# Optimization experiments

Hardware: AMD Instinct MI355X
Metric: run time of the kernel (lower is better)

The kernel has to match this reference:

```python
import jax, jax.numpy as jnp
import numpy as np

P = 8      # patch_size
DIM = 16   # per-head channel dim
HEADS = 4
LN_EPS = 1e-6


def _conv_patch(x, W, b):
    # stride=kernel=P patch conv; SAME degenerates to VALID when H%P==0
    y = jax.lax.conv_general_dilated(
        x, W, window_strides=(P, P), padding='VALID',
        dimension_numbers=('NHWC', 'HWIO', 'NHWC'))
    return y + b


def _proj_heads(x, W, b):
    # b h w (c p0 p1 head) -> b head (h p0) (w p1) c
    y = _conv_patch(x, W, b)
    B, hh, ww, _ = y.shape
    y = y.reshape(B, hh, ww, DIM, P, P, HEADS)
    y = y.transpose(0, 6, 1, 4, 2, 5, 3)            # b head hh p0 ww p1 c
    return y.reshape(B, HEADS, hh * P, ww * P, DIM)


def _to_patch(t):
    # n head (h p1) (w p2) c -> n head c h w p1 p2
    B, hd, H, W, c = t.shape
    t = t.reshape(B, hd, H // P, P, W // P, P, c)
    return t.transpose(0, 1, 6, 2, 4, 3, 5)


def _from_patch(t):
    # n head c h w p1 p2 -> n head (h p1) (w p2) c
    B, hd, c, hh, ww, _, _ = t.shape
    t = t.transpose(0, 1, 3, 5, 4, 6, 2)
    return t.reshape(B, hd, hh * P, ww * P, c)


def setup_inputs() -> dict:
    key = jax.random.key(0)
    ks = jax.random.split(key, 6)
    B, H, W, Cin = 4, 256, 256, 16
    feat = DIM * HEADS * P * P  # 4096
    s_qkv = 0.02
    inp = {
        'x': jax.random.normal(ks[0], (B, H, W, Cin), jnp.float32),
        'Wq': jax.random.normal(ks[1], (P, P, Cin, feat), jnp.float32) * s_qkv,
        'bq': jnp.zeros((feat,), jnp.float32),
        'Wk': jax.random.normal(ks[2], (P, P, Cin, feat), jnp.float32) * s_qkv,
        'bk': jnp.zeros((feat,), jnp.float32),
        'Wv': jax.random.normal(ks[3], (P, P, Cin, feat), jnp.float32) * s_qkv,
        'bv': jnp.zeros((feat,), jnp.float32),
        'ln_scale': jnp.ones((DIM,), jnp.float32),
        'ln_bias': jnp.zeros((DIM,), jnp.float32),
        'Wout': jax.random.normal(ks[4], (P, P, HEADS * DIM, DIM * P * P), jnp.float32) * 0.02,
        'bout': jnp.zeros((DIM * P * P,), jnp.float32),
    }
    return inp


def reference(x, Wq, bq, Wk, bk, Wv, bv, ln_scale, ln_bias, Wout, bout):
    q = _proj_heads(x, Wq, bq)  # [B, heads, H, W, dim]
    k = _proj_heads(x, Wk, bk)
    v = _proj_heads(x, Wv, bv)

    # frequency-domain 'attention': per-8x8-patch rfft2 multiply irfft2
    qf = jnp.fft.rfft2(_to_patch(q))
    kf = jnp.fft.rfft2(_to_patch(k))
    out = jnp.fft.irfft2(qf * kf, s=(P, P))
    out = _from_patch(out)                          # [B, heads, H, W, dim]

    # LayerNorm over channel dim (flax default eps=1e-6, scale+bias)
    mu = out.mean(-1, keepdims=True)
    var = ((out - mu) ** 2).mean(-1, keepdims=True)
    out = (out - mu) * jax.lax.rsqrt(var + LN_EPS) * ln_scale + ln_bias

    out = v * out
    # b head h w c -> b h w (head c)
    B, hd, H, W, c = out.shape
    out = out.transpose(0, 2, 3, 1, 4).reshape(B, H, W, hd * c)

    # output projection (no heads): conv then b h w (c p0 p1) -> b (h p0) (w p1) c
    y = _conv_patch(out, Wout, bout)
    Bo, hh, ww, _ = y.shape
    y = y.reshape(Bo, hh, ww, DIM, P, P).transpose(0, 1, 4, 2, 5, 3)
    return y.reshape(Bo, hh * P, ww * P, DIM)
```

## Files before the change

### kernel.cpp

```cpp
#include <hip/hip_runtime.h>
#include <hip/hip_bf16.h>
#include <cstdint>
#include <cstddef>

typedef float  f32x4  __attribute__((ext_vector_type(4)));
typedef __bf16 bf16x8 __attribute__((ext_vector_type(8)));
typedef __bf16 bf16x4 __attribute__((ext_vector_type(4)));


#define GLOAD_LDS16(gp, lp)                                                     \
    __builtin_amdgcn_global_load_lds(                                           \
        (const __attribute__((address_space(1))) void*)(gp),                    \
        (__attribute__((address_space(3))) void*)(lp), 16, 0, 0)

__global__ __launch_bounds__(256) void k_im2col(const float* __restrict__ x,
                                                __bf16* __restrict__ Xb)
{
    const int p = blockIdx.x;
    const int t = threadIdx.x;
    const int b = p >> 10, hh = (p >> 5) & 31, ww = p & 31;
    const int e = t * 4;
    const int c = e & 15, ij = e >> 4;
    const int i = ij >> 3, j = ij & 7;
    const size_t src = ((((size_t)(b * 256 + hh * 8 + i)) * 256) + (ww * 8 + j)) * 16 + c;
    f32x4 v = *(const f32x4*)(x + src);
    bf16x4 o;
    o[0] = (__bf16)v[0]; o[1] = (__bf16)v[1]; o[2] = (__bf16)v[2]; o[3] = (__bf16)v[3];
    *(bf16x4*)(Xb + (size_t)p * 1024 + e) = o;
}

__global__ __launch_bounds__(256) void k_wqkvT(const float* __restrict__ Wq,
                                               const float* __restrict__ Wk,
                                               const float* __restrict__ Wv,
                                               __bf16* __restrict__ WT)
{
    __shared__ float tile[64][129];
    int q = blockIdx.x;
    const int t = threadIdx.x;
    const int k0 = (q & 7) * 128;  q >>= 3;
    const int ch = q & 15;         q >>= 4;
    const int head = q & 3;
    const int s = q >> 2;
    const float* __restrict__ W = (s == 0) ? Wq : (s == 1) ? Wk : Wv;

#pragma unroll
    for (int rep = 0; rep < 32; rep++) {
        const int idx = rep * 256 + t;
        const int kl = idx >> 6, pp = idx & 63;
        tile[pp][kl] = W[(size_t)(k0 + kl) * 4096 + ch * 256 + pp * 4 + head];
    }
    __syncthreads();
    const size_t nbase = (size_t)s * 4096 + head * 1024 + ch * 64;
#pragma unroll
    for (int rep = 0; rep < 32; rep++) {
        const int idx = rep * 256 + t;
        const int pp = idx >> 7, kl = idx & 127;
        WT[(nbase + pp) * 1024 + k0 + kl] = (__bf16)tile[pp][kl];
    }
}

__global__ __launch_bounds__(256) void k_biasperm(const float* __restrict__ bq,
                                                  const float* __restrict__ bk,
                                                  const float* __restrict__ bv,
                                                  float* __restrict__ bp)
{
    const int n = blockIdx.x * 256 + threadIdx.x;
    const int s = n >> 12;
    const int r = n & 4095;
    const int head = r >> 10, c = (r >> 6) & 15, pp = r & 63;
    const float* __restrict__ b = (s == 0) ? bq : (s == 1) ? bk : bv;
    bp[n] = b[c * 256 + pp * 4 + head];
}

__global__ __launch_bounds__(256) void k_woutT(const float* __restrict__ Wo,
                                               __bf16* __restrict__ WT)
{
    __shared__ float tile[64][129];
    const int q = blockIdx.x;
    const int t = threadIdx.x;
    const int n0 = (q & 15) * 64;
    const int k0 = (q >> 4) * 128;
    const int ch = n0 >> 6;
#pragma unroll
    for (int rep = 0; rep < 32; rep++) {
        const int idx = rep * 256 + t;
        const int kl = idx >> 6, nn = idx & 63;
        tile[nn][kl] = Wo[(size_t)(k0 + kl) * 1024 + n0 + nn];
    }
    __syncthreads();
#pragma unroll
    for (int rep = 0; rep < 32; rep++) {
        const int idx = rep * 256 + t;
        const int nn = idx >> 7, kl = idx & 127;
        const int no = ((nn >> 3) & 7) * 128 + (nn & 7) * 16 + ch;
        WT[(size_t)no * 4096 + k0 + kl] = (__bf16)tile[nn][kl];
    }
}

template <int BN, int EPI>
__global__ __launch_bounds__(256, 3) void gemm_glds(const __bf16* __restrict__ A,
                                                    const __bf16* __restrict__ Bt,
                                                    void* __restrict__ Cout,
                                                    const float* __restrict__ bias,
                                                    const int M, const int N,
                                                    const int K, const int nbx)
{
    constexpr int BM  = 128, BK = 64;
    constexpr int NF  = BN / 32;
    constexpr int APW = (BM * BK / 512) / 4;
    constexpr int BPW = (BN * BK / 512) / 4;
    __shared__ __bf16 As[BM * BK];
    __shared__ __bf16 Bs[BN * BK];

    const int t = threadIdx.x;
    const int l = t & 63, w = t >> 6;

    const int nwg  = (int)gridDim.x;
    const int cpx  = nwg >> 3;
    const int bid  = (int)blockIdx.x;
    const int sbid = (bid & 7) * cpx + (bid >> 3);
    const int bm = sbid / nbx, bn = sbid - bm * nbx;
    const int row0 = bm * BM, col0 = bn * BN;

    const int wr = w >> 1, wc = w & 1;
    const int lr = l & 15;
    const int lk = (l >> 4) * 8;
    const int srow = l >> 3;
    const int scol = (l & 7) * 8;

    f32x4 acc[4][NF] = {};

    for (int k0 = 0; k0 < K; k0 += BK) {
        __syncthreads();
#pragma unroll
        for (int p = 0; p < APW; p++) {
            const int chunk = w * APW + p;
            const __bf16* gp = A + (size_t)(row0 + chunk * 8 + srow) * K + k0 + scol;
            GLOAD_LDS16(gp, &As[chunk * 512]);
        }
#pragma unroll
        for (int p = 0; p < BPW; p++) {
            const int chunk = w * BPW + p;
            const __bf16* gp = Bt + (size_t)(col0 + chunk * 8 + srow) * K + k0 + scol;
            GLOAD_LDS16(gp, &Bs[chunk * 512]);
        }
        __syncthreads();
#pragma unroll
        for (int kk = 0; kk < 2; kk++) {
            bf16x8 af[4], bfr[NF];
#pragma unroll
            for (int m = 0; m < 4; m++)
                af[m] = *(const bf16x8*)&As[(wr * 64 + m * 16 + lr) * BK + kk * 32 + lk];
#pragma unroll
            for (int n = 0; n < NF; n++)
                bfr[n] = *(const bf16x8*)&Bs[(wc * (BN / 2) + n * 16 + lr) * BK + kk * 32 + lk];
#pragma unroll
            for (int m = 0; m < 4; m++)
#pragma unroll
                for (int n = 0; n < NF; n++)
                    acc[m][n] = __builtin_amdgcn_mfma_f32_16x16x32_bf16(
                        af[m], bfr[n], acc[m][n], 0, 0, 0);
        }
    }

    const int rbase = row0 + wr * 64;
    const int cbase = col0 + wc * (BN / 2);
    if (EPI == 0) {
        __bf16* __restrict__ C = (__bf16*)Cout;
#pragma unroll
        for (int m = 0; m < 4; m++)
#pragma unroll
            for (int n = 0; n < NF; n++) {
                const int cw = cbase + n * 16 + lr;
                const float bsv = bias[cw];
#pragma unroll
                for (int j = 0; j < 4; j++) {
                    const int rw = rbase + m * 16 + (l >> 4) * 4 + j;
                    C[(size_t)rw * N + cw] = (__bf16)(acc[m][n][j] + bsv);
                }
            }
    } else {
        float* __restrict__ Y = (float*)Cout;
#pragma unroll
        for (int m = 0; m < 4; m++)
#pragma unroll
            for (int n = 0; n < NF; n++) {
                const int cw = cbase + n * 16 + lr;
                const float bsv = bias[((cw & 15) << 6) + ((cw >> 7) << 3) + ((cw >> 4) & 7)];
                const int p0 = cw >> 7, low = cw & 127;
#pragma unroll
                for (int j = 0; j < 4; j++) {
                    const int rw = rbase + m * 16 + (l >> 4) * 4 + j;
                    const int b = rw >> 10, hh = (rw >> 5) & 31, wwp = rw & 31;
                    const size_t addr =
                        (size_t)(b * 256 + hh * 8 + p0) * 4096 + wwp * 128 + low;
                    Y[addr] = acc[m][n][j] + bsv;
                }
            }
    }
}

__global__ __launch_bounds__(128) void k_freqconv(const __bf16* __restrict__ C1,
                                                  const float* __restrict__ lns,
                                                  const float* __restrict__ lnb,
                                                  __bf16* __restrict__ Z)
{
    const int blk = blockIdx.x;
    const int p = blk >> 2, head = blk & 3;
    const int t = threadIdx.x;

    __shared__ float qs[16 * 68];
    __shared__ float ks[16 * 68];
    __shared__ float vs[16 * 68];
    __shared__ float os[16 * 68];

    const __bf16* __restrict__ base = C1 + (size_t)p * 12288 + head * 1024;
    {
        const int cl = t >> 3, off = (t & 7) * 8;
        const bf16x8 vq = *(const bf16x8*)(base + cl * 64 + off);
        const bf16x8 vk = *(const bf16x8*)(base + 4096 + cl * 64 + off);
        const bf16x8 vv = *(const bf16x8*)(base + 8192 + cl * 64 + off);
#pragma unroll
        for (int e = 0; e < 8; e++) {
            qs[cl * 68 + off + e] = (float)vq[e];
            ks[cl * 68 + off + e] = (float)vk[e];
            vs[cl * 68 + off + e] = (float)vv[e];
        }
    }
    __syncthreads();

    const int cc = t >> 3, p0 = t & 7;
    float outr[8] = {0.f, 0.f, 0.f, 0.f, 0.f, 0.f, 0.f, 0.f};
#pragma unroll
    for (int i0 = 0; i0 < 8; i0++) {
        const int kr = (p0 - i0) & 7;
        const f32x4 qa = *(const f32x4*)&qs[cc * 68 + i0 * 8];
        const f32x4 qb = *(const f32x4*)&qs[cc * 68 + i0 * 8 + 4];
        const f32x4 ka = *(const f32x4*)&ks[cc * 68 + kr * 8];
        const f32x4 kb = *(const f32x4*)&ks[cc * 68 + kr * 8 + 4];
        const float qrow[8] = {qa[0], qa[1], qa[2], qa[3], qb[0], qb[1], qb[2], qb[3]};
        const float krow[8] = {ka[0], ka[1], ka[2], ka[3], kb[0], kb[1], kb[2], kb[3]};
#pragma unroll
        for (int j = 0; j < 8; j++) {
            const float qv = qrow[j];
#pragma unroll
            for (int p1 = 0; p1 < 8; p1++)
                outr[p1] = fmaf(qv, krow[(p1 - j) & 7], outr[p1]);
        }
    }
#pragma unroll
    for (int e = 0; e < 8; e++)
        os[cc * 68 + p0 * 8 + e] = outr[e];
    __syncthreads();

    if (t < 64) {
        const int pp = t;
        float o[16];
        float mu = 0.f;
#pragma unroll
        for (int c2 = 0; c2 < 16; c2++) { o[c2] = os[c2 * 68 + pp]; mu += o[c2]; }
        mu *= 0.0625f;
        float var = 0.f;
#pragma unroll
        for (int c2 = 0; c2 < 16; c2++) { const float d = o[c2] - mu; var = fmaf(d, d, var); }
        var *= 0.0625f;
        const float rs = rsqrtf(var + 1e-6f);
        bf16x8 z0, z1;
#pragma unroll
        for (int c2 = 0; c2 < 16; c2++) {
            float zv = (o[c2] - mu) * rs * lns[c2] + lnb[c2];
            zv *= vs[c2 * 68 + pp];
            if (c2 < 8) z0[c2] = (__bf16)zv; else z1[c2 - 8] = (__bf16)zv;
        }
        bf16x8* zp = (bf16x8*)(Z + (size_t)p * 4096 + pp * 64 + head * 16);
        zp[0] = z0;
        zp[1] = z1;
    }
}

extern "C" void kernel_launch(void* const* d_in, const int* in_sizes, int n_in,
                              void* d_out, int out_size, void* d_ws, size_t ws_size,
                              hipStream_t stream)
{
    const float* x   = (const float*)d_in[0];
    const float* Wq  = (const float*)d_in[1];
    const float* bq  = (const float*)d_in[2];
    const float* Wk  = (const float*)d_in[3];
    const float* bk  = (const float*)d_in[4];
    const float* Wv  = (const float*)d_in[5];
    const float* bv  = (const float*)d_in[6];
    const float* lns = (const float*)d_in[7];
    const float* lnb = (const float*)d_in[8];
    const float* Wo  = (const float*)d_in[9];
    const float* bo  = (const float*)d_in[10];
    float* out = (float*)d_out;

    char* ws = (char*)d_ws;
    __bf16* Xb    = (__bf16*)(ws);
    __bf16* WqkvT = (__bf16*)(ws + 8388608);
    float*  bperm = (float*) (ws + 33554432);
    __bf16* WoutT = (__bf16*)(ws + 33603584);
    __bf16* C1    = (__bf16*)(ws + 41992192);
    __bf16* Z     = (__bf16*)(ws + 142655488);

    k_im2col  <<<dim3(4096), dim3(256), 0, stream>>>(x, Xb);
    k_wqkvT   <<<dim3(1536), dim3(256), 0, stream>>>(Wq, Wk, Wv, WqkvT);
    k_biasperm<<<dim3(48),   dim3(256), 0, stream>>>(bq, bk, bv, bperm);
    k_woutT   <<<dim3(512),  dim3(256), 0, stream>>>(Wo, WoutT);

    gemm_glds<128, 0><<<dim3(3072), dim3(256), 0, stream>>>(Xb, WqkvT, (void*)C1, bperm,
                                                            4096, 12288, 1024, 96);

    k_freqconv<<<dim3(16384), dim3(128), 0, stream>>>(C1, lns, lnb, Z);

    gemm_glds<64, 1><<<dim3(512), dim3(256), 0, stream>>>(Z, WoutT, (void*)out, bo,
                                                          4096, 1024, 4096, 16);
}
```

Baseline: 282.6 us.

## Replace QKV projection GEMM with 256x256-tile double-buffered 8-wave kernel

Adds a new GEMM kernel for the QKV projection that uses 256x256 output tiles with 512 threads, double-buffered LDS staged via direct global-to-LDS loads with XOR swizzle, quadrant-wise MFMA scheduling with s_setprio, and an XCD-aware block remap. The larger tile raises arithmetic intensity and reduces global reloads of A and B compared with the 128x128 kernel. In exchange, occupancy drops to one 512-thread block per CU with heavy register use (128 accumulators), and the epilogue writes bf16 scalars with strided stores.

```diff
diff --git a/kernel.cpp b/kernel.cpp
--- a/kernel.cpp
+++ b/kernel.cpp
@@ -12,6 +12,8 @@
     __builtin_amdgcn_global_load_lds(                                           \
         (const __attribute__((address_space(1))) void*)(gp),                    \
         (__attribute__((address_space(3))) void*)(lp), 16, 0, 0)
+
+#define MFMA16(d, a, b) d = __builtin_amdgcn_mfma_f32_16x16x32_bf16(a, b, d, 0, 0, 0)
 
 __global__ __launch_bounds__(256) void k_im2col(const float* __restrict__ x,
                                                 __bf16* __restrict__ Xb)
@@ -95,6 +97,186 @@
         const int no = ((nn >> 3) & 7) * 128 + (nn & 7) * 16 + ch;
         WT[(size_t)no * 4096 + k0 + kl] = (__bf16)tile[nn][kl];
     }
+}
+
+__device__ __forceinline__ void stage_half(const __bf16* __restrict__ mat,
+                                           const int gRow0, const int K,
+                                           const int k0, __bf16* lds, const int t)
+{
+    const int w6 = (t >> 6) << 6;
+#pragma unroll
+    for (int r = 0; r < 2; r++) {
+        const int idx = r * 512 + t;
+        const int row = idx >> 3;
+        const int colb = ((t & 7) << 4) ^ ((row & 7) << 4);
+        const char* gp = (const char*)(mat + (size_t)(gRow0 + row) * K + k0) + colb;
+        GLOAD_LDS16(gp, (char*)lds + (size_t)(r * 512 + w6) * 16);
+    }
+}
+
+__global__ __launch_bounds__(512, 1) void gemm256(const __bf16* __restrict__ A,
+                                                  const __bf16* __restrict__ Bt,
+                                                  __bf16* __restrict__ C,
+                                                  const float* __restrict__ bias,
+                                                  const int M, const int N,
+                                                  const int K, const int nbx)
+{
+    __shared__ __bf16 As[2][256 * 64];
+    __shared__ __bf16 Bs[2][256 * 64];
+
+    const int t = threadIdx.x;
+    const int l = t & 63, w = t >> 6;
+    const int wr = w >> 2, wc = w & 3;
+
+    const int nwg = (int)gridDim.x, cpx = nwg >> 3;
+    const int bid = (int)blockIdx.x;
+    const int sbid = (bid & 7) * cpx + (bid >> 3);
+    const int bm = sbid / nbx, bn = sbid - bm * nbx;
+    const int row0 = bm * 256, col0 = bn * 256;
+
+    const int lrow = l & 15;
+    const int lkb  = (l >> 4) << 4;
+    const int lswz = (l & 7) << 4;
+    const int ce0 = ((0  + lkb) ^ lswz) >> 1;
+    const int ce1 = ((64 + lkb) ^ lswz) >> 1;
+
+    const int arow = wr * 128 + lrow;
+    const int brow = wc * 64 + lrow;
+
+    const int NT = K >> 6;
+    f32x4 acc[8][4] = {};
+
+    stage_half(A,  row0,       K, 0,  As[0],        t);
+    stage_half(A,  row0 + 128, K, 0,  As[0] + 8192, t);
+    stage_half(Bt, col0,       K, 0,  Bs[0],        t);
+    stage_half(Bt, col0 + 128, K, 0,  Bs[0] + 8192, t);
+    stage_half(A,  row0,       K, 64, As[1],        t);
+    stage_half(A,  row0 + 128, K, 64, As[1] + 8192, t);
+    asm volatile("s_waitcnt vmcnt(4)" ::: "memory");
+    __builtin_amdgcn_s_barrier();
+
+    int cur = 0;
+    for (int it = 0; it < NT; ++it) {
+        const __bf16* AsC = As[cur];
+        const __bf16* BsC = Bs[cur];
+        const bool doB = (it + 1 < NT);
+        const bool doA = (it + 2 < NT);
+        const int kB = (it + 1) << 6;
+        const int kA = (it + 2) << 6;
+
+        bf16x8 af[4][2], bfr[2][2];
+
+#pragma unroll
+        for (int mi = 0; mi < 4; ++mi) {
+            const int rr = (arow + mi * 16) * 64;
+            af[mi][0] = *(const bf16x8*)&AsC[rr + ce0];
+            af[mi][1] = *(const bf16x8*)&AsC[rr + ce1];
+        }
+#pragma unroll
+        for (int ni = 0; ni < 2; ++ni) {
+            const int rr = (brow + ni * 16) * 64;
+            bfr[ni][0] = *(const bf16x8*)&BsC[rr + ce0];
+            bfr[ni][1] = *(const bf16x8*)&BsC[rr + ce1];
+        }
+        if (doB) stage_half(Bt, col0, K, kB, Bs[cur ^ 1], t);
+        __builtin_amdgcn_s_barrier();
+        __builtin_amdgcn_s_setprio(1);
+#pragma unroll
+        for (int mi = 0; mi < 4; ++mi)
+#pragma unroll
+            for (int ni = 0; ni < 2; ++ni) {
+                MFMA16(acc[mi][ni], af[mi][0], bfr[ni][0]);
+                MFMA16(acc[mi][ni], af[mi][1], bfr[ni][1]);
+            }
+        __builtin_amdgcn_s_setprio(0);
+        __builtin_amdgcn_s_barrier();
+
+#pragma unroll
+        for (int ni = 0; ni < 2; ++ni) {
+            const int rr = (brow + 32 + ni * 16) * 64;
+            bfr[ni][0] = *(const bf16x8*)&BsC[rr + ce0];
+            bfr[ni][1] = *(const bf16x8*)&BsC[rr + ce1];
+        }
+        if (doB) stage_half(Bt, col0 + 128, K, kB, Bs[cur ^ 1] + 8192, t);
+        __builtin_amdgcn_s_barrier();
+        __builtin_amdgcn_s_setprio(1);
+#pragma unroll
+        for (int mi = 0; mi < 4; ++mi)
+#pragma unroll
+            for (int ni = 0; ni < 2; ++ni) {
+                MFMA16(acc[mi][2 + ni], af[mi][0], bfr[ni][0]);
+                MFMA16(acc[mi][2 + ni], af[mi][1], bfr[ni][1]);
+            }
+        __builtin_amdgcn_s_setprio(0);
+        __builtin_amdgcn_s_barrier();
+
+#pragma unroll
+        for (int mi = 0; mi < 4; ++mi) {
+            const int rr = (arow + 64 + mi * 16) * 64;
+            af[mi][0] = *(const bf16x8*)&AsC[rr + ce0];
+            af[mi][1] = *(const bf16x8*)&AsC[rr + ce1];
+        }
+#pragma unroll
+        for (int ni = 0; ni < 2; ++ni) {
+            const int rr = (brow + ni * 16) * 64;
+            bfr[ni][0] = *(const bf16x8*)&BsC[rr + ce0];
+            bfr[ni][1] = *(const bf16x8*)&BsC[rr + ce1];
+        }
+        __builtin_amdgcn_s_barrier();
+        __builtin_amdgcn_s_setprio(1);
+#pragma unroll
+        for (int mi = 0; mi < 4; ++mi)
+#pragma unroll
+            for (int ni = 0; ni < 2; ++ni) {
+                MFMA16(acc[4 + mi][ni], af[mi][0], bfr[ni][0]);
+                MFMA16(acc[4 + mi][ni], af[mi][1], bfr[ni][1]);
+            }
+        __builtin_amdgcn_s_setprio(0);
+        __builtin_amdgcn_s_barrier();
+
+        if (doA) {
+            stage_half(A, row0,       K, kA, As[cur],        t);
+            stage_half(A, row0 + 128, K, kA, As[cur] + 8192, t);
+        }
+#pragma unroll
+        for (int ni = 0; ni < 2; ++ni) {
+            const int rr = (brow + 32 + ni * 16) * 64;
+            bfr[ni][0] = *(const bf16x8*)&BsC[rr + ce0];
+            bfr[ni][1] = *(const bf16x8*)&BsC[rr + ce1];
+        }
+        __builtin_amdgcn_s_barrier();
+        __builtin_amdgcn_s_setprio(1);
+#pragma unroll
+        for (int mi = 0; mi < 4; ++mi)
+#pragma unroll
+            for (int ni = 0; ni < 2; ++ni) {
+                MFMA16(acc[4 + mi][2 + ni], af[mi][0], bfr[ni][0]);
+                MFMA16(acc[4 + mi][2 + ni], af[mi][1], bfr[ni][1]);
+            }
+        __builtin_amdgcn_s_setprio(0);
+        if (it + 1 < NT) {
+            if (doA) asm volatile("s_waitcnt vmcnt(4)" ::: "memory");
+            else     asm volatile("s_waitcnt vmcnt(0)" ::: "memory");
+            __builtin_amdgcn_s_barrier();
+        }
+        cur ^= 1;
+    }
+
+    const int rbase = row0 + wr * 128;
+    const int cbase = col0 + wc * 64;
+    const int jr = (l >> 4) * 4;
+#pragma unroll
+    for (int m = 0; m < 8; ++m)
+#pragma unroll
+        for (int n = 0; n < 4; ++n) {
+            const int cw = cbase + n * 16 + lrow;
+            const float bsv = bias[cw];
+#pragma unroll
+            for (int j = 0; j < 4; ++j) {
+                const int rw = rbase + m * 16 + jr + j;
+                C[(size_t)rw * N + cw] = (__bf16)(acc[m][n][j] + bsv);
+            }
+        }
 }
 
 template <int BN, int EPI>
@@ -308,8 +490,8 @@
     k_biasperm<<<dim3(48),   dim3(256), 0, stream>>>(bq, bk, bv, bperm);
     k_woutT   <<<dim3(512),  dim3(256), 0, stream>>>(Wo, WoutT);
 
-    gemm_glds<128, 0><<<dim3(3072), dim3(256), 0, stream>>>(Xb, WqkvT, (void*)C1, bperm,
-                                                            4096, 12288, 1024, 96);
+    gemm256<<<dim3(768), dim3(512), 0, stream>>>(Xb, WqkvT, C1, bperm,
+                                                 4096, 12288, 1024, 48);
 
     k_freqconv<<<dim3(16384), dim3(128), 0, stream>>>(C1, lns, lnb, Z);
 
```

After: 257.6 us. 1.1x faster.
